# Kernel tuning notes

Hardware: AMD Instinct MI355X
Metric: run time of the kernel (lower is better)

## Reference

```python
import jax, jax.numpy as jnp
import numpy as np

N, E, B, F, H = 400000, 1600000, 8192, 64, 96


def gcn_conv(x, src, dst, W, b, n):
    # PyG GCNConv: x' = D^-1/2 (A+I) D^-1/2 (x W) + b
    x = x @ W
    loop = jnp.arange(n)
    s = jnp.concatenate([src, loop])
    d = jnp.concatenate([dst, loop])
    deg = jax.ops.segment_sum(jnp.ones_like(d, x.dtype), d, num_segments=n)
    dinv = jnp.where(deg > 0, jax.lax.rsqrt(deg), 0.0)
    norm = dinv[s] * dinv[d]  # [E+N]
    return jax.ops.segment_sum(norm[:, None] * x[s], d, num_segments=n) + b


def forward_convs(x, src, dst, Ws, bs, n):
    for i in range(len(Ws)):
        x = gcn_conv(x, src, dst, Ws[i], bs[i], n)
        if i < len(Ws) - 1:
            x = jax.nn.relu(x)
    return x


def att_pool(x, batch, W1, b1, W2, b2, nb):
    # GlobalAttention: gate = Lin(F,F)->ReLU->Lin(F,1); segment softmax; weighted sum
    g = (jax.nn.relu(x @ W1 + b1) @ W2 + b2)[:, 0]  # [N]
    gmax = jax.ops.segment_max(g, batch, num_segments=nb)
    e = jnp.exp(g - gmax[batch])
    denom = jax.ops.segment_sum(e, batch, num_segments=nb)
    a = e / denom[batch]
    return jax.ops.segment_sum(a[:, None] * x, batch, num_segments=nb)


def mean_pool(x, batch, nb):
    s = jax.ops.segment_sum(x, batch, num_segments=nb)
    cnt = jax.ops.segment_sum(jnp.ones_like(batch, x.dtype), batch, num_segments=nb)
    return s / jnp.maximum(cnt, 1.0)[:, None]


def setup_inputs() -> dict:
    key = jax.random.key(0)
    ks = jax.random.split(key, 32)
    inp = {
        "x_p": jax.random.normal(ks[0], (N, F), jnp.float32),
        "x_d": jax.random.normal(ks[1], (N, F), jnp.float32),
        "edge_attr_p": jax.random.normal(ks[2], (E, 8), jnp.float32),
        "edge_attr_d": jax.random.normal(ks[3], (E, 8), jnp.float32),
        "edge_index_p": jax.random.randint(ks[4], (2, E), 0, N),
        "edge_index_d": jax.random.randint(ks[5], (2, E), 0, N),
        "x_p_batch": jnp.sort(jax.random.randint(ks[6], (N,), 0, B)),
        "x_d_batch": jnp.sort(jax.random.randint(ks[7], (N,), 0, B)),
    }
    def lin(k, fi, fo):
        bnd = 1.0 / np.sqrt(fi)
        k1, k2 = jax.random.split(k)
        return (jax.random.uniform(k1, (fi, fo), jnp.float32, -bnd, bnd),
                jax.random.uniform(k2, (fo,), jnp.float32, -bnd, bnd))
    inp["gate_W1"], inp["gate_b1"] = lin(ks[8], F, F)
    inp["gate_W2"], inp["gate_b2"] = lin(ks[9], F, 1)
    dims = [(F, H), (H, H), (H, H)]
    for side, base in (("p", 10), ("d", 13)):
        for i, (fi, fo) in enumerate(dims):
            W, b = lin(ks[base + i], fi, fo)
            inp[f"conv{side}_W{i}"], inp[f"conv{side}_b{i}"] = W, b
    inp["lin_W0"], inp["lin_b0"] = lin(ks[16], 2 * H + 2 * F, H)
    inp["lin_W1"], inp["lin_b1"] = lin(ks[17], H, 1)
    return inp


def reference(x_p, x_d, edge_attr_p, edge_attr_d, edge_index_p, edge_index_d,
              x_p_batch, x_d_batch, gate_W1, gate_b1, gate_W2, gate_b2,
              convp_W0, convp_b0, convp_W1, convp_b1, convp_W2, convp_b2,
              convd_W0, convd_b0, convd_W1, convd_b1, convd_W2, convd_b2,
              lin_W0, lin_b0, lin_W1, lin_b1):
    n, nb = x_p.shape[0], B
    xp_att = att_pool(x_p, x_p_batch, gate_W1, gate_b1, gate_W2, gate_b2, nb)
    xd_att = att_pool(x_d, x_d_batch, gate_W1, gate_b1, gate_W2, gate_b2, nb)
    xp = forward_convs(x_p, edge_index_p[0], edge_index_p[1],
                       [convp_W0, convp_W1, convp_W2], [convp_b0, convp_b1, convp_b2], n)
    xd = forward_convs(x_d, edge_index_d[0], edge_index_d[1],
                       [convd_W0, convd_W1, convd_W2], [convd_b0, convd_b1, convd_b2], n)
    xp = mean_pool(xp, x_p_batch, nb)
    xd = mean_pool(xd, x_d_batch, nb)
    x = jnp.concatenate([xp, xd, xp_att, xd_att], axis=1)  # [B, 2H+2F]
    # dropout p=0.5 is identity in eval mode
    x = jax.nn.relu(x @ lin_W0 + lin_b0)
    return x @ lin_W1 + lin_b1  # [B, 1]
```

## Files before the change

kernel.cpp:

```cpp
#include <hip/hip_runtime.h>

#define NN 400000
#define EE 1600000
#define NB 8192

typedef float vf4 __attribute__((ext_vector_type(4)));
typedef float vf2 __attribute__((ext_vector_type(2)));

__global__ void k_seg(const int* __restrict__ batch, int* __restrict__ start){
  int b = blockIdx.x*256 + threadIdx.x;
  if (b > NB) return;
  int lo = 0, hi = NN;
  while (lo < hi){ int mid = (lo+hi)>>1; if (batch[mid] < b) lo = mid+1; else hi = mid; }
  start[b] = lo;
}

__global__ __launch_bounds__(256) void k_gate(const float* __restrict__ x,
    const float* __restrict__ W1, const float* __restrict__ b1,
    const float* __restrict__ W2, const float* __restrict__ b2,
    float* __restrict__ g){
  __shared__ __align__(16) float sX[64*68];
  __shared__ __align__(16) float sW[64*64];
  __shared__ float sB[128];
  __shared__ float sRed[64*17];
  const int tid = threadIdx.x;
  const int r0 = blockIdx.x << 6;
  for (int i = tid; i < 4096; i += 256) sW[i] = W1[i];
  if (tid < 64) sB[tid] = b1[tid];
  else if (tid < 128) sB[tid] = W2[tid-64];
  for (int i = tid; i < 4096; i += 256){
    int r = i >> 6, k = i & 63;
    sX[k*68 + r] = x[(size_t)r0*64 + i];
  }
  __syncthreads();
  const int tx = tid & 15;
  const int ty = tid >> 4;
  float acc[4][4];
  #pragma unroll
  for (int i = 0; i < 4; ++i)
    #pragma unroll
    for (int j = 0; j < 4; ++j) acc[i][j] = 0.f;
  for (int k = 0; k < 64; ++k){
    vf4 a = *(const vf4*)&sX[k*68 + ty*4];
    vf4 w = *(const vf4*)&sW[k*64 + tx*4];
    #pragma unroll
    for (int i = 0; i < 4; ++i)
      #pragma unroll
      for (int j = 0; j < 4; ++j)
        acc[i][j] = fmaf(a[i], w[j], acc[i][j]);
  }
  #pragma unroll
  for (int i = 0; i < 4; ++i){
    float p = 0.f;
    #pragma unroll
    for (int j = 0; j < 4; ++j){
      int c = tx*4 + j;
      p = fmaf(fmaxf(acc[i][j] + sB[c], 0.f), sB[64+c], p);
    }
    sRed[(ty*4+i)*17 + tx] = p;
  }
  __syncthreads();
  if (tid < 64){
    float s = 0.f;
    #pragma unroll
    for (int j = 0; j < 16; ++j) s += sRed[tid*17 + j];
    g[r0 + tid] = s + b2[0];
  }
}

__global__ __launch_bounds__(64) void k_att(const float* __restrict__ x, const float* __restrict__ g,
    const int* __restrict__ start, float* __restrict__ att){
  int b = blockIdx.x, lane = threadIdx.x;
  int s0 = start[b], s1 = start[b+1];
  if (s1 <= s0){ att[b*64+lane] = 0.f; return; }
  float m = -3.0e38f;
  for (int i = s0+lane; i < s1; i += 64) m = fmaxf(m, g[i]);
  #pragma unroll
  for (int off = 32; off; off >>= 1) m = fmaxf(m, __shfl_xor(m, off));
  float s = 0.f;
  for (int i = s0+lane; i < s1; i += 64) s += expf(g[i]-m);
  #pragma unroll
  for (int off = 32; off; off >>= 1) s += __shfl_xor(s, off);
  float acc = 0.f;
  for (int i = s0; i < s1; ++i)
    acc = fmaf(expf(g[i]-m), x[(size_t)i*64+lane], acc);
  att[b*64+lane] = acc / s;
}

__global__ void k_zero(int* __restrict__ degI, int* __restrict__ gc){
  int i = blockIdx.x*256 + threadIdx.x;
  if (i < NN) degI[i] = 0;
  if (i == 0) *gc = 0;
}
__global__ void k_count(const int* __restrict__ dst, int* __restrict__ degI){
  int e = blockIdx.x*256 + threadIdx.x;
  if (e < EE) atomicAdd(&degI[dst[e]], 1);
}
__global__ __launch_bounds__(256) void k_alloc(const int* __restrict__ degI, int* __restrict__ gc,
    int* __restrict__ base, int* __restrict__ cursor, float* __restrict__ dinv){
  int i = blockIdx.x*256 + threadIdx.x;
  int lane = threadIdx.x & 63;
  int d = (i < NN) ? degI[i] : 0;
  int incl = d;
  #pragma unroll
  for (int off = 1; off < 64; off <<= 1){
    int t = __shfl_up(incl, off);
    if (lane >= off) incl += t;
  }
  int waveTotal = __shfl(incl, 63);
  int wbase = 0;
  if (lane == 63) wbase = atomicAdd(gc, waveTotal);
  wbase = __shfl(wbase, 63);
  if (i < NN){
    int b = wbase + incl - d;
    base[i] = b; cursor[i] = b;
    dinv[i] = 1.f / sqrtf((float)d + 1.f);
  }
}
__global__ void k_fillcsr(const int* __restrict__ src, const int* __restrict__ dst,
                          const float* __restrict__ dinv,
                          int* __restrict__ cursor, int2* __restrict__ csr2){
  int e = blockIdx.x*256 + threadIdx.x;
  if (e >= EE) return;
  int s = src[e];
  int p = atomicAdd(&cursor[dst[e]], 1);
  csr2[p] = make_int2(s, __float_as_int(dinv[s]));
}

template<int K, bool RELU>
__global__ __launch_bounds__(256) void k_gemm(const float* __restrict__ in,
    const float* __restrict__ W, const float* __restrict__ bias, float* __restrict__ out){
  __shared__ __align__(16) float sIn[K*68];
  __shared__ __align__(16) float sW[K*96];
  __shared__ float sB[96];
  const int tid = threadIdx.x;
  const int r0 = blockIdx.x << 6;
  for (int i = tid; i < K*96; i += 256) sW[i] = W[i];
  if (tid < 96) sB[tid] = bias[tid];
  for (int i = tid; i < 64*K; i += 256){
    int r = i / K, k = i - r*K;
    sIn[k*68 + r] = in[(size_t)r0*K + i];
  }
  __syncthreads();
  const int tx = tid & 15;
  const int ty = tid >> 4;
  float acc[4][6];
  #pragma unroll
  for (int i = 0; i < 4; ++i)
    #pragma unroll
    for (int j = 0; j < 6; ++j) acc[i][j] = 0.f;
  for (int k = 0; k < K; ++k){
    vf4 a   = *(const vf4*)&sIn[k*68 + ty*4];
    vf2 w01 = *(const vf2*)&sW[k*96 + tx*6];
    vf2 w23 = *(const vf2*)&sW[k*96 + tx*6 + 2];
    vf2 w45 = *(const vf2*)&sW[k*96 + tx*6 + 4];
    float w[6] = {w01[0], w01[1], w23[0], w23[1], w45[0], w45[1]};
    #pragma unroll
    for (int i = 0; i < 4; ++i)
      #pragma unroll
      for (int j = 0; j < 6; ++j)
        acc[i][j] = fmaf(a[i], w[j], acc[i][j]);
  }
  #pragma unroll
  for (int i = 0; i < 4; ++i){
    size_t row = r0 + ty*4 + i;
    #pragma unroll
    for (int j = 0; j < 6; ++j){
      float v = acc[i][j] + sB[tx*6 + j];
      if (RELU) v = fmaxf(v, 0.f);
      out[row*96 + tx*6 + j] = v;
    }
  }
}

__global__ __launch_bounds__(256) void k_gemm_pool(const float* __restrict__ in,
    const float* __restrict__ W, const float* __restrict__ bias,
    const int* __restrict__ start, float* __restrict__ out){
  constexpr int K = 96;
  __shared__ __align__(16) float sIn[K*68];
  __shared__ __align__(16) float sW[K*96];
  __shared__ float sB[96];
  const int tid = threadIdx.x;
  const int r0 = blockIdx.x << 6;
  for (int i = tid; i < K*96; i += 256) sW[i] = W[i];
  if (tid < 96) sB[tid] = bias[tid];
  for (int i = tid; i < 64*K; i += 256){
    int r = i / K, k = i - r*K;
    sIn[k*68 + r] = in[(size_t)r0*K + i];
  }
  __syncthreads();
  const int tx = tid & 15;
  const int ty = tid >> 4;
  float acc[4][6];
  #pragma unroll
  for (int i = 0; i < 4; ++i)
    #pragma unroll
    for (int j = 0; j < 6; ++j) acc[i][j] = 0.f;
  for (int k = 0; k < K; ++k){
    vf4 a   = *(const vf4*)&sIn[k*68 + ty*4];
    vf2 w01 = *(const vf2*)&sW[k*96 + tx*6];
    vf2 w23 = *(const vf2*)&sW[k*96 + tx*6 + 2];
    vf2 w45 = *(const vf2*)&sW[k*96 + tx*6 + 4];
    float w[6] = {w01[0], w01[1], w23[0], w23[1], w45[0], w45[1]};
    #pragma unroll
    for (int i = 0; i < 4; ++i)
      #pragma unroll
      for (int j = 0; j < 6; ++j)
        acc[i][j] = fmaf(a[i], w[j], acc[i][j]);
  }
  #pragma unroll
  for (int i = 0; i < 4; ++i){
    int row = r0 + ty*4 + i;
    bool nz = start[row+1] > start[row];
    #pragma unroll
    for (int j = 0; j < 6; ++j){
      float v = nz ? (acc[i][j] + sB[tx*6 + j]) : 0.f;
      out[(size_t)row*96 + tx*6 + j] = v;
    }
  }
}

__global__ __launch_bounds__(256) void k_gather96(const float* __restrict__ xw,
    const int2* __restrict__ csr2, const int* __restrict__ base, const int* __restrict__ degI,
    const float* __restrict__ dinv, float* __restrict__ out){
  const int grp  = threadIdx.x >> 5;
  const int lane = threadIdx.x & 31;
  const int i = (blockIdx.x << 3) + grp;
  const bool act = lane < 24;
  const vf4* __restrict__ xw4 = (const vf4*)xw;
  const float di = dinv[i];
  const int b0 = base[i], cnt = degI[i];
  vf4 s = {0.f,0.f,0.f,0.f};
  if (act) s = di * xw4[(size_t)i*24 + lane];
  for (int t = 0; t < cnt; t += 8){
    int2 e[8]; float w[8];
    #pragma unroll
    for (int k = 0; k < 8; ++k){
      int p = t + k;
      int q = p < cnt ? p : cnt-1;
      e[k] = csr2[b0 + q];
      w[k] = (p < cnt) ? __int_as_float(e[k].y) : 0.f;
    }
    if (act){
      #pragma unroll
      for (int k = 0; k < 8; ++k){
        vf4 v = xw4[(size_t)e[k].x*24 + lane];
        s += w[k]*v;
      }
    }
  }
  if (act){
    vf4 r = di * s;
    ((vf4*)out)[(size_t)i*24 + lane] = r;
  }
}

__global__ __launch_bounds__(256) void k_gather64(const float* __restrict__ x,
    const int2* __restrict__ csr2, const int* __restrict__ base, const int* __restrict__ degI,
    const float* __restrict__ dinv, float* __restrict__ out){
  const int grp  = threadIdx.x >> 4;
  const int lane = threadIdx.x & 15;
  const int i = (blockIdx.x << 4) + grp;
  const vf4* __restrict__ x4 = (const vf4*)x;
  const float di = dinv[i];
  const int b0 = base[i], cnt = degI[i];
  vf4 s = di * x4[(size_t)i*16 + lane];
  for (int t = 0; t < cnt; t += 8){
    int2 e[8]; float w[8];
    #pragma unroll
    for (int k = 0; k < 8; ++k){
      int p = t + k;
      int q = p < cnt ? p : cnt-1;
      e[k] = csr2[b0 + q];
      w[k] = (p < cnt) ? __int_as_float(e[k].y) : 0.f;
    }
    #pragma unroll
    for (int k = 0; k < 8; ++k){
      vf4 v = x4[(size_t)e[k].x*16 + lane];
      s += w[k]*v;
    }
  }
  vf4 r = di * s;
  ((vf4*)out)[(size_t)i*16 + lane] = r;
}

__global__ __launch_bounds__(128) void k_mean(const float* __restrict__ h,
    const int* __restrict__ start, float* __restrict__ mean){
  int b = blockIdx.x, f = threadIdx.x;
  if (f >= 96) return;
  int s0 = start[b], s1 = start[b+1];
  float acc = 0.f;
  for (int i = s0; i < s1; ++i) acc += h[(size_t)i*96+f];
  mean[b*96+f] = acc / fmaxf((float)(s1-s0), 1.f);
}

__global__ __launch_bounds__(128) void k_final(const float* __restrict__ meanP, const float* __restrict__ meanD,
    const float* __restrict__ attP, const float* __restrict__ attD,
    const float* __restrict__ W0, const float* __restrict__ b0,
    const float* __restrict__ W1, const float* __restrict__ b1,
    float* __restrict__ out){
  __shared__ float cat[320];
  __shared__ float hb[96];
  int b = blockIdx.x, tid = threadIdx.x;
  if (tid < 96){ cat[tid] = meanP[b*96+tid]; cat[96+tid] = meanD[b*96+tid]; }
  if (tid < 64){ cat[192+tid] = attP[b*64+tid]; cat[256+tid] = attD[b*64+tid]; }
  __syncthreads();
  if (tid < 96){
    float acc = b0[tid];
    for (int k = 0; k < 320; ++k) acc = fmaf(cat[k], W0[k*96+tid], acc);
    hb[tid] = fmaxf(acc, 0.f) * W1[tid];
  }
  __syncthreads();
  if (tid == 0){
    float y = b1[0];
    for (int j = 0; j < 96; ++j) y += hb[j];
    out[b] = y;
  }
}

extern "C" void kernel_launch(void* const* d_in, const int* in_sizes, int n_in,
                              void* d_out, int out_size, void* d_ws, size_t ws_size,
                              hipStream_t stream){
  const float* x_p = (const float*)d_in[0];
  const float* x_d = (const float*)d_in[1];
  const int* ei_p = (const int*)d_in[4];
  const int* ei_d = (const int*)d_in[5];
  const int* batch_p = (const int*)d_in[6];
  const int* batch_d = (const int*)d_in[7];
  const float* gW1 = (const float*)d_in[8];
  const float* gb1 = (const float*)d_in[9];
  const float* gW2 = (const float*)d_in[10];
  const float* gb2 = (const float*)d_in[11];
  const float* cW[2][3] = {{(const float*)d_in[12],(const float*)d_in[14],(const float*)d_in[16]},
                           {(const float*)d_in[18],(const float*)d_in[20],(const float*)d_in[22]}};
  const float* cB[2][3] = {{(const float*)d_in[13],(const float*)d_in[15],(const float*)d_in[17]},
                           {(const float*)d_in[19],(const float*)d_in[21],(const float*)d_in[23]}};
  const float* lW0 = (const float*)d_in[24];
  const float* lb0 = (const float*)d_in[25];
  const float* lW1 = (const float*)d_in[26];
  const float* lb1 = (const float*)d_in[27];
  float* out = (float*)d_out;

  float* fws = (float*)d_ws;
  size_t off = 0;
  float* A     = fws + off; off += (size_t)NN*96;
  float* Bf    = fws + off; off += (size_t)NN*96;
  float* dinv  = fws + off; off += NN;
  float* g     = fws + off; off += NN;
  float* attP  = fws + off; off += (size_t)NB*64;
  float* attD  = fws + off; off += (size_t)NB*64;
  float* meanP = fws + off; off += (size_t)NB*96;
  float* meanD = fws + off; off += (size_t)NB*96;
  float* poolT = fws + off; off += (size_t)NB*96;
  int2* csr2  = (int2*)(fws + off);
  int* iws = (int*)(csr2 + EE);
  int* segP   = iws;             iws += NB+1;
  int* segD   = iws;             iws += NB+1;
  int* degI   = iws;             iws += NN;
  int* base   = iws;             iws += NN;
  int* cursor = iws;             iws += NN;
  int* gc     = iws;             iws += 1;

  k_seg<<<(NB+1+255)/256, 256, 0, stream>>>(batch_p, segP);
  k_seg<<<(NB+1+255)/256, 256, 0, stream>>>(batch_d, segD);

  for (int side = 0; side < 2; ++side){
    const float* x  = side ? x_d : x_p;
    const int* src = side ? ei_d : ei_p;
    const int* dst = src + EE;
    const int* seg = side ? segD : segP;
    float* att  = side ? attD : attP;
    float* mean = side ? meanD : meanP;

    k_gate<<<NN/64, 256, 0, stream>>>(x, gW1, gb1, gW2, gb2, g);
    k_att<<<NB, 64, 0, stream>>>(x, g, seg, att);

    k_zero   <<<(NN+255)/256, 256, 0, stream>>>(degI, gc);
    k_count  <<<(EE+255)/256, 256, 0, stream>>>(dst, degI);
    k_alloc  <<<(NN+255)/256, 256, 0, stream>>>(degI, gc, base, cursor, dinv);
    k_fillcsr<<<(EE+255)/256, 256, 0, stream>>>(src, dst, dinv, cursor, csr2);

    k_gather64<<<NN/16, 256, 0, stream>>>(x, csr2, base, degI, dinv, A);
    k_gemm<64,true ><<<NN/64, 256, 0, stream>>>(A, cW[side][0], cB[side][0], Bf);
    k_gather96<<<NN/8, 256, 0, stream>>>(Bf, csr2, base, degI, dinv, A);
    k_gemm<96,true ><<<NN/64, 256, 0, stream>>>(A, cW[side][1], cB[side][1], Bf);
    k_gather96<<<NN/8, 256, 0, stream>>>(Bf, csr2, base, degI, dinv, A);
    k_mean<<<NB, 128, 0, stream>>>(A, seg, poolT);
    k_gemm_pool<<<NB/64, 256, 0, stream>>>(poolT, cW[side][2], cB[side][2], seg, mean);
  }
  k_final<<<NB, 128, 0, stream>>>(meanP, meanD, attP, attD, lW0, lb0, lW1, lb1, out);
}
```

Measured before the change: 2.285 ms.

## Fuse last GCN aggregation with per-graph mean pooling

The final neighbour gather and the mean-pool kernel are merged into one kernel with one block per graph. Each block aggregates its nodes' neighbourhoods, reduces them in shared memory, and writes only the pooled row. This removes the write and re-read of the full N×96 intermediate and one launch. In exchange, parallelism is per graph, with 8 warps per block over about 49 nodes, so load balance and occupancy may be worse than the per-node gather.

```diff
diff --git a/kernel.cpp b/kernel.cpp
--- a/kernel.cpp
+++ b/kernel.cpp
@@ -255,6 +255,51 @@
   }
 }
 
+__global__ __launch_bounds__(256) void k_poolgather(const float* __restrict__ h,
+    const int2* __restrict__ csr2, const int* __restrict__ base, const int* __restrict__ degI,
+    const float* __restrict__ dinv, const int* __restrict__ start, float* __restrict__ poolT){
+  __shared__ __align__(16) float sAcc[8][96];
+  const int b = blockIdx.x;
+  const int s0 = start[b], s1 = start[b+1];
+  const int grp = threadIdx.x >> 5, lane = threadIdx.x & 31;
+  const bool act = lane < 24;
+  const vf4* __restrict__ h4 = (const vf4*)h;
+  vf4 acc = {0.f,0.f,0.f,0.f};
+  for (int i = s0 + grp; i < s1; i += 8){
+    const float di = dinv[i];
+    const int b0 = base[i], cnt = degI[i];
+    vf4 s = {0.f,0.f,0.f,0.f};
+    if (act) s = di * h4[(size_t)i*24 + lane];
+    for (int t = 0; t < cnt; t += 8){
+      int2 e[8]; float w[8];
+      #pragma unroll
+      for (int k = 0; k < 8; ++k){
+        int p = t + k;
+        int q = p < cnt ? p : cnt-1;
+        e[k] = csr2[b0 + q];
+        w[k] = (p < cnt) ? __int_as_float(e[k].y) : 0.f;
+      }
+      if (act){
+        #pragma unroll
+        for (int k = 0; k < 8; ++k){
+          vf4 v = h4[(size_t)e[k].x*24 + lane];
+          s += w[k]*v;
+        }
+      }
+    }
+    acc += di * s;
+  }
+  if (act) *(vf4*)&sAcc[grp][lane*4] = acc;
+  __syncthreads();
+  const int tid = threadIdx.x;
+  if (tid < 96){
+    float v = 0.f;
+    #pragma unroll
+    for (int g = 0; g < 8; ++g) v += sAcc[g][tid];
+    poolT[(size_t)b*96 + tid] = v / fmaxf((float)(s1 - s0), 1.f);
+  }
+}
+
 __global__ __launch_bounds__(256) void k_gather64(const float* __restrict__ x,
     const int2* __restrict__ csr2, const int* __restrict__ base, const int* __restrict__ degI,
     const float* __restrict__ dinv, float* __restrict__ out){
@@ -282,16 +327,6 @@
   }
   vf4 r = di * s;
   ((vf4*)out)[(size_t)i*16 + lane] = r;
-}
-
-__global__ __launch_bounds__(128) void k_mean(const float* __restrict__ h,
-    const int* __restrict__ start, float* __restrict__ mean){
-  int b = blockIdx.x, f = threadIdx.x;
-  if (f >= 96) return;
-  int s0 = start[b], s1 = start[b+1];
-  float acc = 0.f;
-  for (int i = s0; i < s1; ++i) acc += h[(size_t)i*96+f];
-  mean[b*96+f] = acc / fmaxf((float)(s1-s0), 1.f);
 }
 
 __global__ __launch_bounds__(128) void k_final(const float* __restrict__ meanP, const float* __restrict__ meanD,
@@ -384,8 +419,7 @@
     k_gemm<64,true ><<<NN/64, 256, 0, stream>>>(A, cW[side][0], cB[side][0], Bf);
     k_gather96<<<NN/8, 256, 0, stream>>>(Bf, csr2, base, degI, dinv, A);
     k_gemm<96,true ><<<NN/64, 256, 0, stream>>>(A, cW[side][1], cB[side][1], Bf);
-    k_gather96<<<NN/8, 256, 0, stream>>>(Bf, csr2, base, degI, dinv, A);
-    k_mean<<<NB, 128, 0, stream>>>(A, seg, poolT);
+    k_poolgather<<<NB, 256, 0, stream>>>(Bf, csr2, base, degI, dinv, seg, poolT);
     k_gemm_pool<<<NB/64, 256, 0, stream>>>(poolT, cW[side][2], cB[side][2], seg, mean);
   }
   k_final<<<NB, 128, 0, stream>>>(meanP, meanD, attP, attD, lW0, lb0, lW1, lb1, out);
```

Measured after the change: 2.127 ms. -6.9%, faster.
